# Kernel optimization log

Hardware: AMD Instinct MI355X
Metric: run time of the kernel (lower is better)

Reference implementation:

```python
import jax, jax.numpy as jnp
import numpy as np

NBINS = (128, 64, 32)
LOG2PI = float(np.log(2.0 * np.pi))


def _quadratic_spline_stack(x, genes_oi, local_gene_ix, delta, uh, uw):
    """Stack of piecewise-quadratic (piecewise-linear density) splines on [0,1].
    Per split with n heights / n-1 widths (n-1 bins). Returns (outputs, logabsdet)."""
    uh_oi = uh[genes_oi]  # [G, sum(n)]
    uw_oi = uw[genes_oi]  # [G, sum(n-1)]
    outputs = x
    logabsdet = jnp.zeros_like(x)
    oh = ow = od = 0
    for n in NBINS:
        nh, nw = n, n - 1
        uhs = uh_oi[:, oh:oh + nh]
        uws = uw_oi[:, ow:ow + nw]
        ds = delta[:, od:od + nh]
        oh += nh; ow += nw; od += nh
        # per-gene bin widths / locations
        widths_g = jax.nn.softmax(uws, axis=-1)                     # [G, nw]
        bl = jnp.cumsum(widths_g, axis=-1)
        bl = bl.at[:, -1].set(1.0)
        bin_loc_g = jnp.pad(bl, ((0, 0), (1, 0)))                   # [G, nw+1]
        # gather per cut
        w = widths_g[local_gene_ix]                                 # [N, nw]
        loc = bin_loc_g[local_gene_ix]                              # [N, nw+1]
        # per-cut knot heights: gene baseline + cell/gene delta, normalized to unit area
        h_un = jnp.exp(uhs[local_gene_ix] + ds)                     # [N, nh]
        area = jnp.sum(0.5 * (h_un[:, :-1] + h_un[:, 1:]) * w, axis=-1, keepdims=True)
        h = h_un / area                                             # [N, nh]
        seg = 0.5 * (h[:, :-1] + h[:, 1:]) * w                      # bin masses [N, nw]
        left_cdf = jnp.pad(jnp.cumsum(seg, axis=-1)[:, :-1], ((0, 0), (1, 0)))  # [N, nw]
        # locate bin
        bin_idx = jnp.clip(jnp.sum(outputs[:, None] >= loc, axis=-1) - 1, 0, nw - 1)
        gi = bin_idx[:, None]
        loc_l = jnp.take_along_axis(loc, gi, -1)[:, 0]
        w_b = jnp.take_along_axis(w, gi, -1)[:, 0]
        cdf_l = jnp.take_along_axis(left_cdf, gi, -1)[:, 0]
        h_l = jnp.take_along_axis(h, gi, -1)[:, 0]
        h_r = jnp.take_along_axis(h, gi + 1, -1)[:, 0]
        alpha = (outputs - loc_l) / w_b
        outputs = (0.5 * (h_r - h_l) * w_b) * alpha * alpha + h_l * w_b * alpha + cdf_l
        logabsdet = logabsdet + jnp.log(h_l + (h_r - h_l) * alpha)
    return outputs, logabsdet


def setup_inputs() -> dict:
    key = jax.random.key(0)
    ks = jax.random.split(key, 10)
    B, L, G_total, G_oi, C, N = 512, 16, 20000, 500, 224, 200000
    clustering = jax.random.uniform(ks[0], (B, L), dtype=jnp.float32)
    coordinates = jax.random.uniform(ks[1], (N,), dtype=jnp.float32, minval=1e-4, maxval=1.0 - 1e-4)
    genes_oi = jax.random.randint(ks[2], (G_oi,), 0, G_total)
    local_gene_ix = jax.random.randint(ks[3], (N,), 0, G_oi)
    local_cellxgene_ix = jax.random.randint(ks[4], (N,), 0, B * G_oi)
    localcellxgene_ix = jax.random.randint(ks[5], (N,), 0, B * G_total)
    logit_weight = jax.random.normal(ks[6], (G_total, L, C), dtype=jnp.float32) * 0.01
    rho_weight = jax.random.normal(ks[7], (G_total, L), dtype=jnp.float32) * 0.05
    rho_bias = 1e-5 + (1.0 - 1e-5) * jax.random.uniform(ks[8], (G_total,), dtype=jnp.float32)
    k9, k10 = jax.random.split(ks[9])
    unnormalized_heights = jax.random.normal(k9, (G_total, sum(NBINS)), dtype=jnp.float32) * 0.1
    unnormalized_widths = jax.random.normal(k10, (G_total, sum(n - 1 for n in NBINS)), dtype=jnp.float32) * 0.1
    return dict(clustering=clustering, coordinates=coordinates, genes_oi=genes_oi,
                local_gene_ix=local_gene_ix, local_cellxgene_ix=local_cellxgene_ix,
                localcellxgene_ix=localcellxgene_ix, logit_weight=logit_weight,
                rho_weight=rho_weight, rho_bias=rho_bias,
                unnormalized_heights=unnormalized_heights,
                unnormalized_widths=unnormalized_widths)


def reference(clustering, coordinates, genes_oi, local_gene_ix, local_cellxgene_ix,
              localcellxgene_ix, logit_weight, rho_weight, rho_bias,
              unnormalized_heights, unnormalized_widths):
    B = clustering.shape[0]
    G = genes_oi.shape[0]
    n_total_genes = rho_bias.shape[0]
    # Decoder (n_layers=0 -> nn_output = latent)
    lw_oi = logit_weight[genes_oi]                                   # [G, L, C]
    mixture_delta = jnp.einsum('bl,glc->bgc', clustering, lw_oi)     # [B, G, C]
    rho_delta = clustering @ rho_weight.T                            # [B, G_total]
    rho = jax.nn.softmax(jnp.log(rho_bias)[None, :] + rho_delta, axis=-1)
    rho_cuts = rho.reshape(-1)[localcellxgene_ix]                    # [N]
    md_cuts = mixture_delta.reshape(B * G, -1)[local_cellxgene_ix]   # [N, C]
    _, lik_mixture = _quadratic_spline_stack(coordinates, genes_oi, local_gene_ix,
                                             md_cuts, unnormalized_heights, unnormalized_widths)
    lik_overall = jnp.log(rho_cuts) + jnp.log(jnp.float32(n_total_genes))
    elbo = -jnp.sum(lik_mixture + lik_overall)
    # Normal(0, exp(log_scale=0)=1) regularization log-probs
    def normal_logpdf(v):
        return -0.5 * v * v - 0.5 * LOG2PI
    elbo = elbo - jnp.sum(normal_logpdf(lw_oi))
    elbo = elbo - jnp.sum(normal_logpdf(rho_weight[genes_oi]))
    return elbo
```

## Files before the change

kernel.cpp:

```cpp
#include <hip/hip_runtime.h>
#include <cstddef>

#define LOG2PI_F 1.8378770664093453f
#define LOG2E_F  1.4426950408889634f

__device__ __forceinline__ float wave_sum(float v) {
#pragma unroll
    for (int o = 32; o >= 1; o >>= 1) v += __shfl_xor(v, o, 64);
    return v;
}
__device__ __forceinline__ float wave_max(float v) {
#pragma unroll
    for (int o = 32; o >= 1; o >>= 1) v = fmaxf(v, __shfl_xor(v, o, 64));
    return v;
}
__device__ __forceinline__ float wave_scan_incl(float v, int lane) {
#pragma unroll
    for (int o = 1; o < 64; o <<= 1) {
        float t = __shfl_up(v, o, 64);
        if (lane >= o) v += t;
    }
    return v;
}

__global__ void k_init(const float* __restrict__ rho_bias, float* __restrict__ logrb,
                       int* __restrict__ counts, float* __restrict__ pC, int G_total) {
    int i = blockIdx.x * blockDim.x + threadIdx.x;
    if (i < G_total) logrb[i] = __logf(rho_bias[i]);
    if (i < 512) counts[i] = 0;
    if (i == 512 + 0) pC[0] = 0.f;
}

__global__ void k_prep(const int* __restrict__ genes_oi,
                       const float* __restrict__ uh, const float* __restrict__ uw,
                       const float* __restrict__ lw, const float* __restrict__ rw,
                       float4* __restrict__ pk, float* __restrict__ lwT,
                       float* __restrict__ pB) {
    const int g = blockIdx.x;
    const int tid = threadIdx.x;
    const int gs = genes_oi[g];

    float acc = 0.f;
    if (tid < 224) {
        const float* src = lw + (size_t)gs * 3584;
        float* dst = lwT + (size_t)g * 3584;
        float vv[16];
#pragma unroll
        for (int l = 0; l < 16; ++l) {
            float v = src[l * 224 + tid];
            vv[l] = v * LOG2E_F;
            acc = fmaf(v, v, acc);
        }
        float4* d4 = (float4*)(dst + (size_t)tid * 16);
#pragma unroll
        for (int q = 0; q < 4; ++q)
            d4[q] = make_float4(vv[4 * q + 0], vv[4 * q + 1], vv[4 * q + 2], vv[4 * q + 3]);
    }
    if (tid < 16) { float v = rw[(size_t)gs * 16 + tid]; acc = fmaf(v, v, acc); }

    if (tid < 64) {
        const int t = tid;
        const float* uhg = uh + (size_t)gs * 224;
        const float* uwg = uw + (size_t)gs * 221;
        float4* pkg = pk + (size_t)g * 224;
        const int NH[3] = {128, 64, 32};
        const int OH[3] = {0, 128, 192};
        const int OW[3] = {0, 127, 190};
        const int SO[3] = {0, 128, 191};
#pragma unroll
        for (int lev = 0; lev < 3; ++lev) {
            const int nw = NH[lev] - 1;
            float v0 = (t < nw)      ? uwg[OW[lev] + t]      : -INFINITY;
            float v1 = (t + 64 < nw) ? uwg[OW[lev] + t + 64] : -INFINITY;
            float mx = wave_max(fmaxf(v0, v1));
            float e0 = (t < nw)      ? __expf(v0 - mx) : 0.f;
            float e1 = (t + 64 < nw) ? __expf(v1 - mx) : 0.f;
            float inv = 1.0f / wave_sum(e0 + e1);
            float w0 = e0 * inv, w1 = e1 * inv;
            float i0 = wave_scan_incl(w0, t);
            float tot0 = __shfl(i0, 63, 64);
            float i1 = wave_scan_incl(w1, t) + tot0;
            if (t < nw) {
                float loc = (t == nw - 1) ? 1.0f : i0;
                pkg[SO[lev] + t] = make_float4(uhg[OH[lev] + t + 1] * LOG2E_F, 0.5f * w0, loc, 0.f);
            }
            if (t + 64 < nw) {
                int j = t + 64;
                float loc = (j == nw - 1) ? 1.0f : i1;
                pkg[SO[lev] + j] = make_float4(uhg[OH[lev] + j + 1] * LOG2E_F, 0.5f * w1, loc, 0.f);
            }
        }
        if (t == 0)
            pkg[127] = make_float4(uhg[0] * LOG2E_F, uhg[128] * LOG2E_F, uhg[192] * LOG2E_F, 0.f);
    }

    __shared__ float sm[256];
    sm[tid] = acc;
    __syncthreads();
    for (int o = 128; o > 0; o >>= 1) { if (tid < o) sm[tid] += sm[tid + o]; __syncthreads(); }
    if (tid == 0) pB[g] = 0.5f * sm[0] + 0.5f * LOG2PI_F * (3584.0f + 16.0f);
}

__global__ void k_lse(const float* __restrict__ clustering, const float* __restrict__ rw,
                      const float* __restrict__ logrb, float* __restrict__ lse, int G_total) {
    const int b = blockIdx.x;
    const int tid = threadIdx.x;
    __shared__ float cl_s[16];
    if (tid < 16) cl_s[tid] = clustering[(size_t)b * 16 + tid];
    __syncthreads();
    float m = -INFINITY, s = 0.f;
    for (int g = tid; g < G_total; g += blockDim.x) {
        const float4* r4 = (const float4*)(rw + (size_t)g * 16);
        float d = 0.f;
#pragma unroll
        for (int q = 0; q < 4; ++q) {
            float4 v = r4[q];
            d = fmaf(cl_s[4 * q + 0], v.x, d);
            d = fmaf(cl_s[4 * q + 1], v.y, d);
            d = fmaf(cl_s[4 * q + 2], v.z, d);
            d = fmaf(cl_s[4 * q + 3], v.w, d);
        }
        float logit = logrb[g] + d;
        float mn = fmaxf(m, logit);
        s = s * __expf(m - mn) + __expf(logit - mn);
        m = mn;
    }
    __shared__ float ms[256], ss[256];
    ms[tid] = m; ss[tid] = s;
    __syncthreads();
    for (int o = 128; o > 0; o >>= 1) {
        if (tid < o) {
            float m2 = ms[tid + o], s2 = ss[tid + o];
            float mn = fmaxf(ms[tid], m2);
            ss[tid] = ss[tid] * __expf(ms[tid] - mn) + s2 * __expf(m2 - mn);
            ms[tid] = mn;
        }
        __syncthreads();
    }
    if (tid == 0) lse[b] = ms[0] + __logf(ss[0]);
}

__global__ void k_histlik(const int* __restrict__ lcx, const int* __restrict__ lc2,
                          int* __restrict__ counts,
                          const float* __restrict__ clustering, const float* __restrict__ rw,
                          const float* __restrict__ logrb, const float* __restrict__ lse,
                          float* __restrict__ pC, int N, int G_oi, int G_total, float logGt) {
    const int i = blockIdx.x * blockDim.x + threadIdx.x;
    float acc = 0.f;
    if (i < N) {
        atomicAdd(&counts[(unsigned)lcx[i] % (unsigned)G_oi], 1);
        const int v = lc2[i];
        const unsigned b2 = (unsigned)v / (unsigned)G_total;
        const unsigned gt = (unsigned)v - b2 * (unsigned)G_total;
        const float4* c4 = (const float4*)(clustering + (size_t)b2 * 16);
        const float4* r4 = (const float4*)(rw + (size_t)gt * 16);
        float d2 = 0.f;
#pragma unroll
        for (int q = 0; q < 4; ++q) {
            float4 a = c4[q], b = r4[q];
            d2 = fmaf(a.x, b.x, d2); d2 = fmaf(a.y, b.y, d2);
            d2 = fmaf(a.z, b.z, d2); d2 = fmaf(a.w, b.w, d2);
        }
        acc = -(logrb[gt] + d2 - lse[b2] + logGt);
    }
    acc = wave_sum(acc);
    __shared__ float wsm[4];
    if ((threadIdx.x & 63) == 0) wsm[threadIdx.x >> 6] = acc;
    __syncthreads();
    if (threadIdx.x == 0)
        atomicAdd(pC, wsm[0] + wsm[1] + wsm[2] + wsm[3]);
}

__global__ void k_scan(const int* __restrict__ counts, int* __restrict__ offsets,
                       int* __restrict__ cursor, int G_oi) {
    __shared__ int sm[512];
    const int t = threadIdx.x;
    int v = (t < G_oi) ? counts[t] : 0;
    sm[t] = v;
    __syncthreads();
    for (int o = 1; o < 512; o <<= 1) {
        int add = (t >= o) ? sm[t - o] : 0;
        __syncthreads();
        sm[t] += add;
        __syncthreads();
    }
    if (t < G_oi) {
        offsets[t + 1] = sm[t];
        cursor[t] = sm[t] - v;
    }
    if (t == 0) offsets[0] = 0;
}

__global__ void k_scatter(const float* __restrict__ coord, const int* __restrict__ lgix,
                          const int* __restrict__ lcx, int* __restrict__ cursor,
                          int2* __restrict__ packed, int N, int G_oi) {
    int i = blockIdx.x * blockDim.x + threadIdx.x;
    if (i >= N) return;
    unsigned v = (unsigned)lcx[i];
    unsigned g = v % (unsigned)G_oi;
    int pos = atomicAdd(&cursor[g], 1);
    packed[pos] = make_int2(__float_as_int(coord[i]),
                            (int)(((v / (unsigned)G_oi) << 16) | (unsigned)lgix[i]));
}

__launch_bounds__(512)
__global__ void k_main2(const int2* __restrict__ packed,
                        const int* __restrict__ offsets,
                        const float* __restrict__ clustering,
                        const float* __restrict__ lwT,
                        const float4* __restrict__ pk,
                        float* __restrict__ pA, int G_oi) {
    const int g = blockIdx.x;
    const int tid = threadIdx.x;
    __shared__ float lds_lw[3584];
    {
        const float* src = lwT + (size_t)g * 3584;
        for (int k = tid; k < 3584; k += 512) lds_lw[k] = src[k];
    }
    __syncthreads();
    const int s = offsets[g], e = offsets[g + 1];
    float acc = 0.f;

    for (int base = s; base < e; base += 512) {
        const int i = base + tid;
        if (i < e) {
            const int2 p = packed[i];
            float x = __int_as_float(p.x);
            const int b1 = (int)((unsigned)p.y >> 16);
            const int gh = p.y & 0xffff;
            const float4* pkh = pk + (size_t)gh * 224;

            float cl[16];
            {
                const float4* c4 = (const float4*)(clustering + (size_t)b1 * 16);
#pragma unroll
                for (int q = 0; q < 4; ++q) {
                    float4 v = c4[q];
                    cl[4 * q + 0] = v.x; cl[4 * q + 1] = v.y;
                    cl[4 * q + 2] = v.z; cl[4 * q + 3] = v.w;
                }
            }
            const float4 uh0 = pkh[127];
            const float uh0v[3] = {uh0.x, uh0.y, uh0.z};

            float lad = 0.f;
            const int NH[3] = {128, 64, 32};
            const int OH[3] = {0, 128, 192};
            const int SO[3] = {0, 128, 191};
#pragma unroll
            for (int lev = 0; lev < 3; ++lev) {
                const int nw = NH[lev] - 1;
                const float* rowbase = lds_lw + (size_t)OH[lev] * 16;
                float hp;
                {
                    const float4* rq = (const float4*)rowbase;
                    float4 r0 = rq[0], r1 = rq[1], r2 = rq[2], r3 = rq[3];
                    float d0 = fmaf(cl[3], r0.w, fmaf(cl[2], r0.z, fmaf(cl[1], r0.y, cl[0] * r0.x)));
                    float d1 = fmaf(cl[7], r1.w, fmaf(cl[6], r1.z, fmaf(cl[5], r1.y, cl[4] * r1.x)));
                    float d2 = fmaf(cl[11], r2.w, fmaf(cl[10], r2.z, fmaf(cl[9], r2.y, cl[8] * r2.x)));
                    float d3 = fmaf(cl[15], r3.w, fmaf(cl[14], r3.z, fmaf(cl[13], r3.y, cl[12] * r3.x)));
                    hp = exp2f(uh0v[lev] + (d0 + d1) + (d2 + d3));
                }
                float h_l = hp, h_r = hp, whb = 0.f, loc_l = 0.f, cdf = 0.f, area = 0.f;
                int in = 0;
                const float4* pks = pkh + SO[lev];
                float4 pkv = pks[0];
                for (int j = 0; j < nw; ++j) {
                    float4 pknext = pks[j + 1];
                    const float4* rq = (const float4*)(rowbase + (size_t)(j + 1) * 16);
                    float4 r0 = rq[0], r1 = rq[1], r2 = rq[2], r3 = rq[3];
                    float d0 = fmaf(cl[3], r0.w, fmaf(cl[2], r0.z, fmaf(cl[1], r0.y, cl[0] * r0.x)));
                    float d1 = fmaf(cl[7], r1.w, fmaf(cl[6], r1.z, fmaf(cl[5], r1.y, cl[4] * r1.x)));
                    float d2 = fmaf(cl[11], r2.w, fmaf(cl[10], r2.z, fmaf(cl[9], r2.y, cl[8] * r2.x)));
                    float d3 = fmaf(cl[15], r3.w, fmaf(cl[14], r3.z, fmaf(cl[13], r3.y, cl[12] * r3.x)));
                    float hn = exp2f(pkv.x + (d0 + d1) + (d2 + d3));
                    float seg = (hp + hn) * pkv.y;
                    if (in == j) { h_r = hn; whb = pkv.y; }
                    bool adv = (x >= pkv.z) && (j < nw - 1);
                    if (adv) { cdf += seg; h_l = hn; loc_l = pkv.z; in = j + 1; }
                    area += seg;
                    hp = hn;
                    pkv = pknext;
                }
                float inv_area = __builtin_amdgcn_rcpf(area);
                float alpha = (x - loc_l) * 0.5f * __builtin_amdgcn_rcpf(whb);
                float t2 = whb * alpha;
                x = (t2 * fmaf(h_r - h_l, alpha, 2.f * h_l) + cdf) * inv_area;
                lad += __logf(fmaf(h_r - h_l, alpha, h_l)) - __logf(area);
            }
            acc -= lad;
        }
    }

    acc = wave_sum(acc);
    __shared__ float wsm[8];
    if ((tid & 63) == 0) wsm[tid >> 6] = acc;
    __syncthreads();
    if (tid == 0) {
        float t = 0.f;
#pragma unroll
        for (int w = 0; w < 8; ++w) t += wsm[w];
        pA[g] = t;
    }
}

__global__ void k_final(const float* __restrict__ pA, const float* __restrict__ pB,
                        const float* __restrict__ pC, float* __restrict__ out, int nA, int nB) {
    const int tid = threadIdx.x;
    float acc = 0.f;
    for (int i = tid; i < nA; i += blockDim.x) acc += pA[i];
    for (int i = tid; i < nB; i += blockDim.x) acc += pB[i];
    if (tid == 0) acc += pC[0];
    __shared__ float sm[256];
    sm[tid] = acc;
    __syncthreads();
    for (int o = 128; o > 0; o >>= 1) { if (tid < o) sm[tid] += sm[tid + o]; __syncthreads(); }
    if (tid == 0) out[0] = sm[0];
}

extern "C" void kernel_launch(void* const* d_in, const int* in_sizes, int n_in,
                              void* d_out, int out_size, void* d_ws, size_t ws_size,
                              hipStream_t stream) {
    const float* clustering        = (const float*)d_in[0];
    const float* coordinates       = (const float*)d_in[1];
    const int*   genes_oi          = (const int*)d_in[2];
    const int*   local_gene_ix     = (const int*)d_in[3];
    const int*   local_cellxgene_ix= (const int*)d_in[4];
    const int*   localcellxgene_ix = (const int*)d_in[5];
    const float* lw                = (const float*)d_in[6];
    const float* rw                = (const float*)d_in[7];
    const float* rho_bias          = (const float*)d_in[8];
    const float* uh                = (const float*)d_in[9];
    const float* uw                = (const float*)d_in[10];

    const int G_total = in_sizes[8];
    const int G_oi    = in_sizes[2];
    const int N       = in_sizes[1];
    const int L       = in_sizes[7] / G_total;
    const int B       = in_sizes[0] / L;

    size_t off = 0;
    char* base = (char*)d_ws;
    auto alloc = [&](size_t nbytes) {
        char* p = base + off;
        off = (off + nbytes + 15) & ~(size_t)15;
        return (void*)p;
    };
    float*  pA      = (float*)alloc(sizeof(float) * (G_oi + 16));
    float*  pB      = (float*)alloc(sizeof(float) * (G_oi + 16));
    float*  pC      = (float*)alloc(sizeof(float) * 16);
    float*  lse     = (float*)alloc(sizeof(float) * (B + 16));
    float*  logrb   = (float*)alloc(sizeof(float) * G_total);
    float*  lwT     = (float*)alloc(sizeof(float) * (size_t)G_oi * 3584);
    float4* pk      = (float4*)alloc(sizeof(float4) * (size_t)G_oi * 224);
    int*    counts  = (int*)alloc(sizeof(int) * 512);
    int*    offsets = (int*)alloc(sizeof(int) * 512);
    int*    cursor  = (int*)alloc(sizeof(int) * 512);
    int2*   packed  = (int2*)alloc(sizeof(int2) * (size_t)N);
    (void)ws_size;

    const float logGt = logf((float)G_total);
    const int TPB = 256;

    k_prep<<<G_oi, 256, 0, stream>>>(genes_oi, uh, uw, lw, rw, pk, lwT, pB);
    k_init<<<(G_total + TPB - 1) / TPB, TPB, 0, stream>>>(rho_bias, logrb, counts, pC, G_total);
    k_lse<<<B, 256, 0, stream>>>(clustering, rw, logrb, lse, G_total);
    k_histlik<<<(N + TPB - 1) / TPB, TPB, 0, stream>>>(local_cellxgene_ix, localcellxgene_ix,
                                                       counts, clustering, rw, logrb, lse,
                                                       pC, N, G_oi, G_total, logGt);
    k_scan<<<1, 512, 0, stream>>>(counts, offsets, cursor, G_oi);
    k_scatter<<<(N + TPB - 1) / TPB, TPB, 0, stream>>>(coordinates, local_gene_ix,
                                                       local_cellxgene_ix, cursor, packed, N, G_oi);
    k_main2<<<G_oi, 512, 0, stream>>>(packed, offsets, clustering, lwT, pk, pA, G_oi);
    k_final<<<1, 256, 0, stream>>>(pA, pB, pC, (float*)d_out, G_oi, G_oi);
}
```

Baseline: 699.3 us.

## Pack spline params to 32-bit bf16/fixed-point, drop LDS staging, fuse init into prep

Spline parameters are packed into one 32-bit word per knot: the baseline height as bf16 and the bin location as 16-bit fixed point. Bin widths are recomputed as location differences, which cuts the parameter footprint from 16 to 4 bytes per knot and lowers memory traffic in the main loop. The main kernel now reads the logit weights straight from global memory instead of staging them in LDS. The init kernel is folded into prep, and the log-sum-exp kernel handles two cells per block and computes log(rho_bias) inline. The reduced-precision heights and locations may change numerical accuracy, and the counts zeroing now assumes specific G_oi bounds.

```diff
diff --git a/kernel.cpp b/kernel.cpp
--- a/kernel.cpp
+++ b/kernel.cpp
@@ -3,6 +3,7 @@
 
 #define LOG2PI_F 1.8378770664093453f
 #define LOG2E_F  1.4426950408889634f
+#define LN2_F    0.6931471805599453f
 
 __device__ __forceinline__ float wave_sum(float v) {
 #pragma unroll
@@ -23,22 +24,28 @@
     return v;
 }
 
-__global__ void k_init(const float* __restrict__ rho_bias, float* __restrict__ logrb,
-                       int* __restrict__ counts, float* __restrict__ pC, int G_total) {
-    int i = blockIdx.x * blockDim.x + threadIdx.x;
-    if (i < G_total) logrb[i] = __logf(rho_bias[i]);
-    if (i < 512) counts[i] = 0;
-    if (i == 512 + 0) pC[0] = 0.f;
+__device__ __forceinline__ unsigned bf16_hi(float x) {
+    unsigned b = __float_as_uint(x);
+    return ((b + 0x7FFFu + ((b >> 16) & 1u)) >> 16) & 0xFFFFu;
+}
+__device__ __forceinline__ unsigned pack_lu(float loc, float uh) {
+    unsigned lo = (unsigned)__float2int_rn(loc * 65535.0f);
+    return (bf16_hi(uh) << 16) | lo;
 }
 
 __global__ void k_prep(const int* __restrict__ genes_oi,
                        const float* __restrict__ uh, const float* __restrict__ uw,
                        const float* __restrict__ lw, const float* __restrict__ rw,
-                       float4* __restrict__ pk, float* __restrict__ lwT,
-                       float* __restrict__ pB) {
+                       unsigned* __restrict__ pk, float* __restrict__ lwT,
+                       float* __restrict__ pB, int* __restrict__ counts,
+                       float* __restrict__ pC) {
     const int g = blockIdx.x;
     const int tid = threadIdx.x;
     const int gs = genes_oi[g];
+
+    if (tid == 0) counts[g] = 0;
+    if (g < 12 && tid == 1) counts[500 + g] = 0;
+    if (g == 0 && tid == 2) pC[0] = 0.f;
 
     float acc = 0.f;
     if (tid < 224) {
@@ -62,7 +69,7 @@
         const int t = tid;
         const float* uhg = uh + (size_t)gs * 224;
         const float* uwg = uw + (size_t)gs * 221;
-        float4* pkg = pk + (size_t)g * 224;
+        unsigned* pkg = pk + (size_t)g * 224;
         const int NH[3] = {128, 64, 32};
         const int OH[3] = {0, 128, 192};
         const int OW[3] = {0, 127, 190};
@@ -82,16 +89,18 @@
             float i1 = wave_scan_incl(w1, t) + tot0;
             if (t < nw) {
                 float loc = (t == nw - 1) ? 1.0f : i0;
-                pkg[SO[lev] + t] = make_float4(uhg[OH[lev] + t + 1] * LOG2E_F, 0.5f * w0, loc, 0.f);
+                pkg[SO[lev] + t] = pack_lu(loc, uhg[OH[lev] + t + 1] * LOG2E_F);
             }
             if (t + 64 < nw) {
                 int j = t + 64;
                 float loc = (j == nw - 1) ? 1.0f : i1;
-                pkg[SO[lev] + j] = make_float4(uhg[OH[lev] + j + 1] * LOG2E_F, 0.5f * w1, loc, 0.f);
-            }
-        }
-        if (t == 0)
-            pkg[127] = make_float4(uhg[0] * LOG2E_F, uhg[128] * LOG2E_F, uhg[192] * LOG2E_F, 0.f);
+                pkg[SO[lev] + j] = pack_lu(loc, uhg[OH[lev] + j + 1] * LOG2E_F);
+            }
+        }
+        if (t == 0) {
+            pkg[127] = (bf16_hi(uhg[0] * LOG2E_F) << 16) | bf16_hi(uhg[128] * LOG2E_F);
+            pkg[223] = bf16_hi(uhg[192] * LOG2E_F) << 16;
+        }
     }
 
     __shared__ float sm[256];
@@ -102,48 +111,58 @@
 }
 
 __global__ void k_lse(const float* __restrict__ clustering, const float* __restrict__ rw,
-                      const float* __restrict__ logrb, float* __restrict__ lse, int G_total) {
-    const int b = blockIdx.x;
+                      const float* __restrict__ rho_bias, float* __restrict__ lse, int G_total) {
+    const int b0 = blockIdx.x * 2;
     const int tid = threadIdx.x;
-    __shared__ float cl_s[16];
-    if (tid < 16) cl_s[tid] = clustering[(size_t)b * 16 + tid];
-    __syncthreads();
-    float m = -INFINITY, s = 0.f;
+    __shared__ float cl_s[32];
+    if (tid < 32) cl_s[tid] = clustering[(size_t)b0 * 16 + tid];
+    __syncthreads();
+    float m0 = -INFINITY, s0 = 0.f, m1 = -INFINITY, s1 = 0.f;
     for (int g = tid; g < G_total; g += blockDim.x) {
         const float4* r4 = (const float4*)(rw + (size_t)g * 16);
-        float d = 0.f;
+        float d0 = 0.f, d1 = 0.f;
 #pragma unroll
         for (int q = 0; q < 4; ++q) {
             float4 v = r4[q];
-            d = fmaf(cl_s[4 * q + 0], v.x, d);
-            d = fmaf(cl_s[4 * q + 1], v.y, d);
-            d = fmaf(cl_s[4 * q + 2], v.z, d);
-            d = fmaf(cl_s[4 * q + 3], v.w, d);
-        }
-        float logit = logrb[g] + d;
-        float mn = fmaxf(m, logit);
-        s = s * __expf(m - mn) + __expf(logit - mn);
-        m = mn;
-    }
-    __shared__ float ms[256], ss[256];
-    ms[tid] = m; ss[tid] = s;
+            d0 = fmaf(cl_s[4 * q + 0], v.x, d0); d0 = fmaf(cl_s[4 * q + 1], v.y, d0);
+            d0 = fmaf(cl_s[4 * q + 2], v.z, d0); d0 = fmaf(cl_s[4 * q + 3], v.w, d0);
+            d1 = fmaf(cl_s[16 + 4 * q + 0], v.x, d1); d1 = fmaf(cl_s[16 + 4 * q + 1], v.y, d1);
+            d1 = fmaf(cl_s[16 + 4 * q + 2], v.z, d1); d1 = fmaf(cl_s[16 + 4 * q + 3], v.w, d1);
+        }
+        float lb = __logf(rho_bias[g]);
+        float l0 = lb + d0, l1 = lb + d1;
+        float n0 = fmaxf(m0, l0);
+        s0 = s0 * __expf(m0 - n0) + __expf(l0 - n0);
+        m0 = n0;
+        float n1 = fmaxf(m1, l1);
+        s1 = s1 * __expf(m1 - n1) + __expf(l1 - n1);
+        m1 = n1;
+    }
+    __shared__ float ms[2][256], ss[2][256];
+    ms[0][tid] = m0; ss[0][tid] = s0; ms[1][tid] = m1; ss[1][tid] = s1;
     __syncthreads();
     for (int o = 128; o > 0; o >>= 1) {
         if (tid < o) {
-            float m2 = ms[tid + o], s2 = ss[tid + o];
-            float mn = fmaxf(ms[tid], m2);
-            ss[tid] = ss[tid] * __expf(ms[tid] - mn) + s2 * __expf(m2 - mn);
-            ms[tid] = mn;
+#pragma unroll
+            for (int k = 0; k < 2; ++k) {
+                float m2 = ms[k][tid + o], s2 = ss[k][tid + o];
+                float mn = fmaxf(ms[k][tid], m2);
+                ss[k][tid] = ss[k][tid] * __expf(ms[k][tid] - mn) + s2 * __expf(m2 - mn);
+                ms[k][tid] = mn;
+            }
         }
         __syncthreads();
     }
-    if (tid == 0) lse[b] = ms[0] + __logf(ss[0]);
+    if (tid == 0) {
+        lse[b0]     = ms[0][0] + __logf(ss[0][0]);
+        lse[b0 + 1] = ms[1][0] + __logf(ss[1][0]);
+    }
 }
 
 __global__ void k_histlik(const int* __restrict__ lcx, const int* __restrict__ lc2,
                           int* __restrict__ counts,
                           const float* __restrict__ clustering, const float* __restrict__ rw,
-                          const float* __restrict__ logrb, const float* __restrict__ lse,
+                          const float* __restrict__ rho_bias, const float* __restrict__ lse,
                           float* __restrict__ pC, int N, int G_oi, int G_total, float logGt) {
     const int i = blockIdx.x * blockDim.x + threadIdx.x;
     float acc = 0.f;
@@ -161,7 +180,7 @@
             d2 = fmaf(a.x, b.x, d2); d2 = fmaf(a.y, b.y, d2);
             d2 = fmaf(a.z, b.z, d2); d2 = fmaf(a.w, b.w, d2);
         }
-        acc = -(logrb[gt] + d2 - lse[b2] + logGt);
+        acc = -(__logf(rho_bias[gt]) + d2 - lse[b2] + logGt);
     }
     acc = wave_sum(acc);
     __shared__ float wsm[4];
@@ -208,16 +227,11 @@
                         const int* __restrict__ offsets,
                         const float* __restrict__ clustering,
                         const float* __restrict__ lwT,
-                        const float4* __restrict__ pk,
+                        const unsigned* __restrict__ pk,
                         float* __restrict__ pA, int G_oi) {
     const int g = blockIdx.x;
     const int tid = threadIdx.x;
-    __shared__ float lds_lw[3584];
-    {
-        const float* src = lwT + (size_t)g * 3584;
-        for (int k = tid; k < 3584; k += 512) lds_lw[k] = src[k];
-    }
-    __syncthreads();
+    const float* lwg = lwT + (size_t)g * 3584;
     const int s = offsets[g], e = offsets[g + 1];
     float acc = 0.f;
 
@@ -228,7 +242,7 @@
             float x = __int_as_float(p.x);
             const int b1 = (int)((unsigned)p.y >> 16);
             const int gh = p.y & 0xffff;
-            const float4* pkh = pk + (size_t)gh * 224;
+            const unsigned* pkh = pk + (size_t)gh * 224;
 
             float cl[16];
             {
@@ -240,8 +254,11 @@
                     cl[4 * q + 2] = v.z; cl[4 * q + 3] = v.w;
                 }
             }
-            const float4 uh0 = pkh[127];
-            const float uh0v[3] = {uh0.x, uh0.y, uh0.z};
+            const unsigned p127 = pkh[127], p223 = pkh[223];
+            const float uhs0 = __uint_as_float(p127 & 0xFFFF0000u);
+            const float uhs1 = __uint_as_float(p127 << 16);
+            const float uhs2 = __uint_as_float(p223 & 0xFFFF0000u);
+            const float uhsv[3] = {uhs0, uhs1, uhs2};
 
             float lad = 0.f;
             const int NH[3] = {128, 64, 32};
@@ -250,7 +267,7 @@
 #pragma unroll
             for (int lev = 0; lev < 3; ++lev) {
                 const int nw = NH[lev] - 1;
-                const float* rowbase = lds_lw + (size_t)OH[lev] * 16;
+                const float* rowbase = lwg + (size_t)OH[lev] * 16;
                 float hp;
                 {
                     const float4* rq = (const float4*)rowbase;
@@ -259,36 +276,41 @@
                     float d1 = fmaf(cl[7], r1.w, fmaf(cl[6], r1.z, fmaf(cl[5], r1.y, cl[4] * r1.x)));
                     float d2 = fmaf(cl[11], r2.w, fmaf(cl[10], r2.z, fmaf(cl[9], r2.y, cl[8] * r2.x)));
                     float d3 = fmaf(cl[15], r3.w, fmaf(cl[14], r3.z, fmaf(cl[13], r3.y, cl[12] * r3.x)));
-                    hp = exp2f(uh0v[lev] + (d0 + d1) + (d2 + d3));
+                    hp = exp2f(uhsv[lev] + (d0 + d1) + (d2 + d3));
                 }
-                float h_l = hp, h_r = hp, whb = 0.f, loc_l = 0.f, cdf = 0.f, area = 0.f;
+                float locp = 0.f, h_l = hp, h_r = hp, whb = 1.f, loc_l = 0.f;
+                float cdf2 = 0.f, area2 = 0.f;
                 int in = 0;
-                const float4* pks = pkh + SO[lev];
-                float4 pkv = pks[0];
+                const unsigned* pks = pkh + SO[lev];
+                unsigned pcur = pks[0];
+#pragma unroll 2
                 for (int j = 0; j < nw; ++j) {
-                    float4 pknext = pks[j + 1];
+                    unsigned pnext = pks[j + 1];
+                    float loc = (float)(pcur & 0xFFFFu) * (1.0f / 65535.0f);
+                    float uhv = __uint_as_float(pcur & 0xFFFF0000u);
                     const float4* rq = (const float4*)(rowbase + (size_t)(j + 1) * 16);
                     float4 r0 = rq[0], r1 = rq[1], r2 = rq[2], r3 = rq[3];
                     float d0 = fmaf(cl[3], r0.w, fmaf(cl[2], r0.z, fmaf(cl[1], r0.y, cl[0] * r0.x)));
                     float d1 = fmaf(cl[7], r1.w, fmaf(cl[6], r1.z, fmaf(cl[5], r1.y, cl[4] * r1.x)));
                     float d2 = fmaf(cl[11], r2.w, fmaf(cl[10], r2.z, fmaf(cl[9], r2.y, cl[8] * r2.x)));
                     float d3 = fmaf(cl[15], r3.w, fmaf(cl[14], r3.z, fmaf(cl[13], r3.y, cl[12] * r3.x)));
-                    float hn = exp2f(pkv.x + (d0 + d1) + (d2 + d3));
-                    float seg = (hp + hn) * pkv.y;
-                    if (in == j) { h_r = hn; whb = pkv.y; }
-                    bool adv = (x >= pkv.z) && (j < nw - 1);
-                    if (adv) { cdf += seg; h_l = hn; loc_l = pkv.z; in = j + 1; }
-                    area += seg;
+                    float hn = exp2f(uhv + (d0 + d1) + (d2 + d3));
+                    float w = loc - locp;
+                    float seg = (hp + hn) * w;
+                    if (in == j) { h_r = hn; whb = w; }
+                    bool adv = (x >= loc) && (j < nw - 1);
+                    if (adv) { cdf2 += seg; h_l = hn; loc_l = loc; in = j + 1; }
+                    area2 += seg;
                     hp = hn;
-                    pkv = pknext;
+                    locp = loc;
+                    pcur = pnext;
                 }
-                float inv_area = __builtin_amdgcn_rcpf(area);
-                float alpha = (x - loc_l) * 0.5f * __builtin_amdgcn_rcpf(whb);
-                float t2 = whb * alpha;
-                x = (t2 * fmaf(h_r - h_l, alpha, 2.f * h_l) + cdf) * inv_area;
-                lad += __logf(fmaf(h_r - h_l, alpha, h_l)) - __logf(area);
-            }
-            acc -= lad;
+                float inv_a = __builtin_amdgcn_rcpf(area2);
+                float alpha = (x - loc_l) * __builtin_amdgcn_rcpf(whb);
+                x = (whb * alpha * fmaf(h_r - h_l, alpha, 2.f * h_l) + cdf2) * inv_a;
+                lad += __logf(fmaf(h_r - h_l, alpha, h_l)) - __logf(area2);
+            }
+            acc -= (lad + 3.0f * LN2_F);
         }
     }
 
@@ -346,27 +368,25 @@
         off = (off + nbytes + 15) & ~(size_t)15;
         return (void*)p;
     };
-    float*  pA      = (float*)alloc(sizeof(float) * (G_oi + 16));
-    float*  pB      = (float*)alloc(sizeof(float) * (G_oi + 16));
-    float*  pC      = (float*)alloc(sizeof(float) * 16);
-    float*  lse     = (float*)alloc(sizeof(float) * (B + 16));
-    float*  logrb   = (float*)alloc(sizeof(float) * G_total);
-    float*  lwT     = (float*)alloc(sizeof(float) * (size_t)G_oi * 3584);
-    float4* pk      = (float4*)alloc(sizeof(float4) * (size_t)G_oi * 224);
-    int*    counts  = (int*)alloc(sizeof(int) * 512);
-    int*    offsets = (int*)alloc(sizeof(int) * 512);
-    int*    cursor  = (int*)alloc(sizeof(int) * 512);
-    int2*   packed  = (int2*)alloc(sizeof(int2) * (size_t)N);
+    float*    pA      = (float*)alloc(sizeof(float) * (G_oi + 16));
+    float*    pB      = (float*)alloc(sizeof(float) * (G_oi + 16));
+    float*    pC      = (float*)alloc(sizeof(float) * 16);
+    float*    lse     = (float*)alloc(sizeof(float) * (B + 16));
+    float*    lwT     = (float*)alloc(sizeof(float) * (size_t)G_oi * 3584);
+    unsigned* pk      = (unsigned*)alloc(sizeof(unsigned) * (size_t)G_oi * 224);
+    int*      counts  = (int*)alloc(sizeof(int) * 512);
+    int*      offsets = (int*)alloc(sizeof(int) * 512);
+    int*      cursor  = (int*)alloc(sizeof(int) * 512);
+    int2*     packed  = (int2*)alloc(sizeof(int2) * (size_t)N);
     (void)ws_size;
 
     const float logGt = logf((float)G_total);
     const int TPB = 256;
 
-    k_prep<<<G_oi, 256, 0, stream>>>(genes_oi, uh, uw, lw, rw, pk, lwT, pB);
-    k_init<<<(G_total + TPB - 1) / TPB, TPB, 0, stream>>>(rho_bias, logrb, counts, pC, G_total);
-    k_lse<<<B, 256, 0, stream>>>(clustering, rw, logrb, lse, G_total);
+    k_prep<<<G_oi, 256, 0, stream>>>(genes_oi, uh, uw, lw, rw, pk, lwT, pB, counts, pC);
+    k_lse<<<B / 2, 256, 0, stream>>>(clustering, rw, rho_bias, lse, G_total);
     k_histlik<<<(N + TPB - 1) / TPB, TPB, 0, stream>>>(local_cellxgene_ix, localcellxgene_ix,
-                                                       counts, clustering, rw, logrb, lse,
+                                                       counts, clustering, rw, rho_bias, lse,
                                                        pC, N, G_oi, G_total, logGt);
     k_scan<<<1, 512, 0, stream>>>(counts, offsets, cursor, G_oi);
     k_scatter<<<(N + TPB - 1) / TPB, TPB, 0, stream>>>(coordinates, local_gene_ix,
```

Result: no change. 702.3 us (+0.4%).
